# Kernel optimization log

Hardware: AMD Instinct MI355X
Metric: run time of the kernel (lower is better)

## Reference

```python
import jax, jax.numpy as jnp
import numpy as np

WH, WW = 7, 7
N = WH * WW
DIM = 384
HEADS = 12
NW = 64          # windows per image
B_ = 2048        # batch * NW


def _relative_position_index():
    ch, cw = np.meshgrid(np.arange(WH), np.arange(WW), indexing='ij')
    coords = np.stack([ch, cw]).reshape(2, -1)                      # [2, N]
    rel = coords[:, :, None] - coords[:, None, :]                   # [2, N, N]
    rel = rel.transpose(1, 2, 0)
    rel[:, :, 0] += WH - 1
    rel[:, :, 1] += WW - 1
    rel[:, :, 0] *= 2 * WW - 1
    return jnp.asarray(rel.sum(-1), dtype=jnp.int32)                # [N, N]


def setup_inputs() -> dict:
    key = jax.random.key(0)
    ks = jax.random.split(key, 7)
    return {
        'x': jax.random.normal(ks[0], (B_, N, DIM), dtype=jnp.float32),
        'qkv_w': jax.random.normal(ks[1], (3 * DIM, DIM), dtype=jnp.float32) * 0.02,
        'qkv_b': jax.random.normal(ks[2], (3 * DIM,), dtype=jnp.float32) * 0.02,
        'proj_w': jax.random.normal(ks[3], (DIM, DIM), dtype=jnp.float32) * 0.02,
        'proj_b': jax.random.normal(ks[4], (DIM,), dtype=jnp.float32) * 0.02,
        'bias_table': jax.random.normal(ks[5], ((2 * WH - 1) * (2 * WW - 1), HEADS), dtype=jnp.float32) * 0.02,
        'mask': jax.random.normal(ks[6], (NW, N, N), dtype=jnp.float32),
        'rel_idx': _relative_position_index(),
    }


def reference(x, qkv_w, qkv_b, proj_w, proj_b, bias_table, mask, rel_idx):
    B_, n, C = x.shape
    H = HEADS
    hd = C // H
    scale = hd ** (-0.5)

    qkv = x @ qkv_w.T + qkv_b                                        # [B_, N, 3C]
    qkv = qkv.reshape(B_, n, 3, H, hd).transpose(2, 0, 3, 1, 4)      # [3, B_, H, N, hd]
    q, k, v = qkv[0], qkv[1], qkv[2]

    attn = jnp.einsum('bhqd,bhkd->bhqk', q * scale, k)               # [B_, H, N, N]

    rpb = bias_table[rel_idx.reshape(-1)].reshape(n, n, H)           # gather [N, N, H]
    attn = attn + rpb.transpose(2, 0, 1)[None]                       # [B_, H, N, N]

    nW = mask.shape[0]
    attn = attn.reshape(B_ // nW, nW, H, n, n) + mask[None, :, None]
    attn = attn.reshape(B_, H, n, n)
    attn = jax.nn.softmax(attn, axis=-1)

    out = jnp.einsum('bhqk,bhkd->bhqd', attn, v)                     # [B_, H, N, hd]
    out = out.transpose(0, 2, 1, 3).reshape(B_, n, C)
    return out @ proj_w.T + proj_b
```

## Files before the change

kernel.cpp:

```cpp
#include <hip/hip_runtime.h>
#include <hip/hip_bf16.h>
#include <cstdint>
#include <cstddef>

#define NTOK 49
#define DIM 384
#define KDIM 384
#define HEADS 12
#define HD 32
#define BATCH 2048
#define MROWS (BATCH * NTOK)

typedef unsigned short u16;
typedef __bf16 bf16x8 __attribute__((ext_vector_type(8)));
typedef unsigned short u16x8 __attribute__((ext_vector_type(8)));
typedef float f32x4 __attribute__((ext_vector_type(4)));

__device__ __forceinline__ u16 f2b(float f) {
  union { float f; unsigned u; } v; v.f = f;
  unsigned r = v.u + 0x7fffu + ((v.u >> 16) & 1u);
  return (u16)(r >> 16);
}

__device__ __forceinline__ bf16x8 ld_bf8(const u16* p) {
  u16x8 u = *(const u16x8*)p;
  return __builtin_bit_cast(bf16x8, u);
}

__device__ __forceinline__ void gload_lds16(const void* g, void* l) {
  __builtin_amdgcn_global_load_lds(
      (const __attribute__((address_space(1))) unsigned*)g,
      (__attribute__((address_space(3))) unsigned*)l, 16, 0, 0);
}

__global__ __launch_bounds__(256) void k_prep(const float* __restrict__ x,
                                              u16* __restrict__ xb,
                                              const float* __restrict__ qkv_w,
                                              u16* __restrict__ wqkvb,
                                              const float* __restrict__ proj_w,
                                              u16* __restrict__ wprojb,
                                              const float* __restrict__ bias_table,
                                              const float* __restrict__ mask,
                                              const int* __restrict__ rel_idx,
                                              float* __restrict__ rpbm) {
  int blk = blockIdx.x;
  if (blk < 38208) {
    const float* in;
    u16* out;
    int i;
    if (blk < 37632) {
      in = x; out = xb; i = blk * 256 + threadIdx.x;
    } else if (blk < 38064) {
      in = qkv_w; out = wqkvb; i = (blk - 37632) * 256 + threadIdx.x;
    } else {
      in = proj_w; out = wprojb; i = (blk - 38064) * 256 + threadIdx.x;
    }
    float4 v = ((const float4*)in)[i];
    ushort4 o;
    o.x = f2b(v.x); o.y = f2b(v.y); o.z = f2b(v.z); o.w = f2b(v.w);
    ((ushort4*)out)[i] = o;
  } else {
    int idx = (blk - 38208) * 256 + threadIdx.x;
    int r  = idx & 3;
    int l  = (idx >> 2) & 63;
    int ni = (idx >> 8) & 3;
    int mi = (idx >> 10) & 3;
    int w  = (idx >> 12) & 63;
    int h  = idx >> 18;
    int row = mi * 16 + (l >> 4) * 4 + r;
    int col = ni * 16 + (l & 15);
    float v = -1e30f;
    if (row < NTOK && col < NTOK)
      v = bias_table[rel_idx[row * NTOK + col] * HEADS + h] +
          mask[(w * NTOK + row) * NTOK + col];
    rpbm[idx] = v;
  }
}

template <int OUT_BF16, int NCOLS, int NTN, int GD8>
__global__ __launch_bounds__(512, 4) void k_gemm256(const u16* __restrict__ A,
                                                    const u16* __restrict__ B,
                                                    const float* __restrict__ bias,
                                                    void* __restrict__ Cv) {
  __shared__ u16 sh[36864];
  int bid = blockIdx.x;
  int tile = (bid & 7) * GD8 + (bid >> 3);
  int mt = tile / NTN, nt = tile - mt * NTN;
  long m0 = (long)mt * 256;
  int n0 = nt * 128;
  int tid = threadIdx.x;
  int lane = tid & 63, wid = tid >> 6;
  int wr = (wid >> 1) * 64, wc = (wid & 1) * 64;
  int c = lane & 15, g = lane >> 4;
  int gsw = (g ^ ((c >> 1) & 3)) * 8;

  int srow = wid * 16 + (lane >> 2);
  int scol = ((lane & 3) ^ ((lane >> 3) & 3)) * 8;
  const u16* gA = A + (m0 + srow) * (long)KDIM + scol;
  const u16* gB = B + (long)(n0 + srow) * KDIM + scol;
  int lrow = srow, lseg = (lane & 3) * 8;

  f32x4 acc[4][4] = {};
  bf16x8 af[4], bfr[4];

#define STAGE256(BUF, KT)                                                      \
  {                                                                            \
    u16* As_ = sh + (BUF) * 12288;                                             \
    u16* Bs_ = As_ + 8192;                                                     \
    gload_lds16(gA + (KT), &As_[lrow * 32 + lseg]);                            \
    gload_lds16(gA + (KT) + 128L * KDIM, &As_[(lrow + 128) * 32 + lseg]);      \
    gload_lds16(gB + (KT), &Bs_[lrow * 32 + lseg]);                            \
  }

#define FRAGREAD(BUF)                                                          \
  {                                                                            \
    const u16* As = sh + (BUF) * 12288;                                        \
    const u16* Bs = As + 8192;                                                 \
    _Pragma("unroll") for (int i = 0; i < 4; ++i) {                            \
      af[i]  = ld_bf8(&As[(wr + i * 16 + c) * 32 + gsw]);                      \
      bfr[i] = ld_bf8(&Bs[(wc + i * 16 + c) * 32 + gsw]);                      \
    }                                                                          \
  }

#define MFMA_CL                                                                \
  __builtin_amdgcn_s_setprio(1);                                               \
  _Pragma("unroll") for (int mi = 0; mi < 4; ++mi)                             \
  _Pragma("unroll") for (int ni = 0; ni < 4; ++ni)                             \
      acc[mi][ni] = __builtin_amdgcn_mfma_f32_16x16x32_bf16(                   \
          af[mi], bfr[ni], acc[mi][ni], 0, 0, 0);                              \
  __builtin_amdgcn_s_setprio(0);

#define GITER(T, NV)                                                           \
  {                                                                            \
    MFMA_CL;                                                                   \
    asm volatile("s_waitcnt vmcnt(" #NV ")" ::: "memory");                     \
    __builtin_amdgcn_s_barrier();                                              \
    __builtin_amdgcn_sched_barrier(0);                                         \
    if ((T) + 3 < 12) STAGE256((T) % 3, ((T) + 3) * 32);                       \
    FRAGREAD(((T) + 1) % 3);                                                   \
  }

  STAGE256(0, 0);
  STAGE256(1, 32);
  STAGE256(2, 64);
  asm volatile("s_waitcnt vmcnt(6)" ::: "memory");
  __builtin_amdgcn_s_barrier();
  __builtin_amdgcn_sched_barrier(0);
  FRAGREAD(0);

  GITER(0, 3)  GITER(1, 3)  GITER(2, 3)  GITER(3, 3)
  GITER(4, 3)  GITER(5, 3)  GITER(6, 3)  GITER(7, 3)
  GITER(8, 3)  GITER(9, 3)  GITER(10, 0)
  { MFMA_CL; }
  __builtin_amdgcn_s_barrier();
#undef GITER
#undef MFMA_CL
#undef FRAGREAD
#undef STAGE256

  if (OUT_BF16) {
    u16* C = (u16*)Cv;
#pragma unroll
    for (int mi = 0; mi < 4; ++mi)
#pragma unroll
      for (int ni = 0; ni < 4; ++ni) {
        int col = wc + ni * 16 + c;
        float bv = bias[n0 + col];
#pragma unroll
        for (int r = 0; r < 4; ++r) {
          int row = wr + mi * 16 + g * 4 + r;
          sh[row * 128 + col] = f2b(acc[mi][ni][r] + bv);
        }
      }
    __syncthreads();
#pragma unroll
    for (int rep = 0; rep < 8; ++rep) {
      int idx = rep * 4096 + tid * 8;
      int row = idx >> 7, col = idx & 127;
      *(u16x8*)(C + (m0 + row) * NCOLS + n0 + col) = *(const u16x8*)&sh[idx];
    }
  } else {
    float* C = (float*)Cv;
    float* shf = (float*)sh;
#pragma unroll
    for (int chunk = 0; chunk < 2; ++chunk) {
      __syncthreads();
      if ((wid >> 2) == chunk) {
#pragma unroll
        for (int mi = 0; mi < 4; ++mi)
#pragma unroll
          for (int ni = 0; ni < 4; ++ni) {
            int col = wc + ni * 16 + c;
            float bv = bias[n0 + col];
#pragma unroll
            for (int r = 0; r < 4; ++r) {
              int lr = ((wid >> 1) & 1) * 64 + mi * 16 + g * 4 + r;
              shf[lr * 128 + col] = acc[mi][ni][r] + bv;
            }
          }
      }
      __syncthreads();
#pragma unroll
      for (int rep = 0; rep < 8; ++rep) {
        int idx = rep * 2048 + tid * 4;
        int row = idx >> 7, col = idx & 127;
        *(float4*)(C + (m0 + chunk * 128 + row) * NCOLS + n0 + col) =
            *(const float4*)&shf[idx];
      }
    }
  }
}

__global__ __launch_bounds__(256) void k_attn(const u16* __restrict__ qkv,
                                              const float* __restrict__ rpbm,
                                              u16* __restrict__ attnout) {
  __shared__ u16 P_lds[4][64 * 64];
  __shared__ u16 vT_lds[4][32 * 64];
  int lane = threadIdx.x & 63, wid = threadIdx.x >> 6;
  int blk = blockIdx.x;
  int w = blk / 96;
  int rr = blk - w * 96;
  int j = rr / 3;
  int hb = rr - j * 3;
  int b = j * 64 + w;
  int h = hb * 4 + wid;
  const u16* base = qkv + (size_t)b * (NTOK * 1152);
  int c = lane & 15, g = lane >> 4;

  u16* vt = vT_lds[wid];
  {
    const u16* vbase = base + 2 * DIM + h * HD;
#pragma unroll
    for (int t = 0; t < 4; ++t) {
      int idx = t * 64 + lane;
      int jj = idx >> 2, d0 = (idx & 3) * 8;
      int jr = jj < NTOK ? jj : NTOK - 1;
      u16x8 vv = *(const u16x8*)(vbase + (size_t)jr * 1152 + d0);
#pragma unroll
      for (int dd = 0; dd < 8; ++dd) {
        int d = d0 + dd;
        int byte = (d * 128 + jj * 2) ^ ((d & 7) << 4);
        *(u16*)((char*)vt + byte) = (u16)vv[dd];
      }
    }
  }

  bf16x8 qa[4], kb[4];
#pragma unroll
  for (int mi = 0; mi < 4; ++mi) {
    int row = mi * 16 + c; if (row > NTOK - 1) row = NTOK - 1;
    qa[mi] = ld_bf8(base + (size_t)row * 1152 + h * HD + g * 8);
  }
#pragma unroll
  for (int ni = 0; ni < 4; ++ni) {
    int row = ni * 16 + c; if (row > NTOK - 1) row = NTOK - 1;
    kb[ni] = ld_bf8(base + (size_t)row * 1152 + DIM + h * HD + g * 8);
  }

  f32x4 s[4][4] = {};
#pragma unroll
  for (int mi = 0; mi < 4; ++mi)
#pragma unroll
    for (int ni = 0; ni < 4; ++ni)
      s[mi][ni] = __builtin_amdgcn_mfma_f32_16x16x32_bf16(qa[mi], kb[ni],
                                                          s[mi][ni], 0, 0, 0);

  const float scale = 0.17677669529663687f;
  const f32x4* rp = (const f32x4*)(rpbm + ((size_t)(h * 64 + w)) * 4096);
#pragma unroll
  for (int mi = 0; mi < 4; ++mi)
#pragma unroll
    for (int ni = 0; ni < 4; ++ni) {
      f32x4 rv = rp[(mi * 4 + ni) * 64 + lane];
#pragma unroll
      for (int r = 0; r < 4; ++r)
        s[mi][ni][r] = s[mi][ni][r] * scale + rv[r];
    }

#pragma unroll
  for (int mi = 0; mi < 4; ++mi)
#pragma unroll
    for (int r = 0; r < 4; ++r) {
      float mx = fmaxf(fmaxf(s[mi][0][r], s[mi][1][r]),
                       fmaxf(s[mi][2][r], s[mi][3][r]));
      mx = fmaxf(mx, __shfl_xor(mx, 1));
      mx = fmaxf(mx, __shfl_xor(mx, 2));
      mx = fmaxf(mx, __shfl_xor(mx, 4));
      mx = fmaxf(mx, __shfl_xor(mx, 8));
      float sum = 0.f;
#pragma unroll
      for (int ni = 0; ni < 4; ++ni) {
        float p = __expf(s[mi][ni][r] - mx);
        s[mi][ni][r] = p;
        sum += p;
      }
      sum += __shfl_xor(sum, 1);
      sum += __shfl_xor(sum, 2);
      sum += __shfl_xor(sum, 4);
      sum += __shfl_xor(sum, 8);
      float inv = __builtin_amdgcn_rcpf(sum);
#pragma unroll
      for (int ni = 0; ni < 4; ++ni) s[mi][ni][r] *= inv;
    }

  u16* pl = P_lds[wid];
#pragma unroll
  for (int mi = 0; mi < 4; ++mi)
#pragma unroll
    for (int ni = 0; ni < 4; ++ni) {
      int col = ni * 16 + c;
#pragma unroll
      for (int r = 0; r < 4; ++r) {
        int row = mi * 16 + g * 4 + r;
        int byte = (row * 128 + col * 2) ^ ((row & 7) << 4);
        *(u16*)((char*)pl + byte) = f2b(s[mi][ni][r]);
      }
    }
  asm volatile("s_waitcnt lgkmcnt(0)" ::: "memory");

  f32x4 o[4][2] = {};
#pragma unroll
  for (int ks = 0; ks < 2; ++ks) {
    bf16x8 vb[2];
#pragma unroll
    for (int n2 = 0; n2 < 2; ++n2) {
      int d = n2 * 16 + c;
      int byte = (d * 128 + ks * 64 + g * 16) ^ ((d & 7) << 4);
      vb[n2] = __builtin_bit_cast(bf16x8, *(const u16x8*)((const char*)vt + byte));
    }
#pragma unroll
    for (int mi = 0; mi < 4; ++mi) {
      int row = mi * 16 + c;
      int byte = (row * 128 + ks * 64 + g * 16) ^ ((row & 7) << 4);
      bf16x8 pa = __builtin_bit_cast(bf16x8, *(const u16x8*)((const char*)pl + byte));
#pragma unroll
      for (int n2 = 0; n2 < 2; ++n2)
        o[mi][n2] = __builtin_amdgcn_mfma_f32_16x16x32_bf16(pa, vb[n2],
                                                            o[mi][n2], 0, 0, 0);
    }
  }

  u16* obase = attnout + (size_t)b * (NTOK * DIM) + h * HD;
#pragma unroll
  for (int mi = 0; mi < 4; ++mi)
#pragma unroll
    for (int r = 0; r < 4; ++r) {
      int row = mi * 16 + g * 4 + r;
      if (row < NTOK) {
#pragma unroll
        for (int n2 = 0; n2 < 2; ++n2)
          obase[(size_t)row * DIM + n2 * 16 + c] = f2b(o[mi][n2][r]);
      }
    }
}

extern "C" void kernel_launch(void* const* d_in, const int* in_sizes, int n_in,
                              void* d_out, int out_size, void* d_ws, size_t ws_size,
                              hipStream_t stream) {
  const float* x       = (const float*)d_in[0];
  const float* qkv_w   = (const float*)d_in[1];
  const float* qkv_b   = (const float*)d_in[2];
  const float* proj_w  = (const float*)d_in[3];
  const float* proj_b  = (const float*)d_in[4];
  const float* bias_tb = (const float*)d_in[5];
  const float* mask    = (const float*)d_in[6];
  const int*   rel_idx = (const int*)d_in[7];
  float* out = (float*)d_out;

  char* ws = (char*)d_ws;
  u16*   xb      = (u16*)(ws + 0);
  u16*   wqkvb   = (u16*)(ws + 77070336);
  u16*   wprojb  = (u16*)(ws + 77955072);
  float* rpbm    = (float*)(ws + 78249984);
  u16*   qkv     = (u16*)(ws + 90832896);
  u16*   attnout = (u16*)(ws + 322043904);

  k_prep<<<50496, 256, 0, stream>>>(x, xb, qkv_w, wqkvb, proj_w, wprojb,
                                    bias_tb, mask, rel_idx, rpbm);

  k_gemm256<1, 1152, 9, 441><<<3528, 512, 0, stream>>>(xb, wqkvb, qkv_b,
                                                       (void*)qkv);

  k_attn<<<6144, 256, 0, stream>>>(qkv, rpbm, attnout);

  k_gemm256<0, 384, 3, 147><<<1176, 512, 0, stream>>>(attnout, wprojb, proj_b,
                                                      (void*)out);

  (void)in_sizes; (void)n_in; (void)out_size; (void)ws_size;
}
```

Before: 342.3 us.

## Compute transposed attention scores to cut softmax shuffles and defer normalization

The attention kernel now computes S^T = K·Q^T, so each query's scores sit along a lane's registers rather than across 16 lanes. The row max and sum then need only two cross-lane shuffles instead of four. The precomputed bias+mask tensor is stored transposed to match. Probabilities are packed to bf16 with v_cvt_pk_bf16_f32 and written as 8-byte LDS stores, and the 1/sum normalization moves to after the PV product, where it is applied once per output element. The PV MFMA is reoriented as V^T·P^T, so output stores become scattered 2-byte writes along the head dimension.

Result: no change. 341.7 us (-0.2%).

```diff
diff --git a/kernel.cpp b/kernel.cpp
--- a/kernel.cpp
+++ b/kernel.cpp
@@ -67,12 +67,12 @@
     int mi = (idx >> 10) & 3;
     int w  = (idx >> 12) & 63;
     int h  = idx >> 18;
-    int row = mi * 16 + (l >> 4) * 4 + r;
-    int col = ni * 16 + (l & 15);
+    int kk = mi * 16 + (l >> 4) * 4 + r;
+    int qq = ni * 16 + (l & 15);
     float v = -1e30f;
-    if (row < NTOK && col < NTOK)
-      v = bias_table[rel_idx[row * NTOK + col] * HEADS + h] +
-          mask[(w * NTOK + row) * NTOK + col];
+    if (kk < NTOK && qq < NTOK)
+      v = bias_table[rel_idx[qq * NTOK + kk] * HEADS + h] +
+          mask[(w * NTOK + qq) * NTOK + kk];
     rpbm[idx] = v;
   }
 }
@@ -212,7 +212,7 @@
 }
 
 __global__ __launch_bounds__(256) void k_attn(const u16* __restrict__ qkv,
-                                              const float* __restrict__ rpbm,
+                                              const float* __restrict__ rpbmT,
                                               u16* __restrict__ attnout) {
   __shared__ u16 P_lds[4][64 * 64];
   __shared__ u16 vT_lds[4][32 * 64];
@@ -245,111 +245,115 @@
     }
   }
 
-  bf16x8 qa[4], kb[4];
+  bf16x8 kf[4], qf[4];
 #pragma unroll
   for (int mi = 0; mi < 4; ++mi) {
     int row = mi * 16 + c; if (row > NTOK - 1) row = NTOK - 1;
-    qa[mi] = ld_bf8(base + (size_t)row * 1152 + h * HD + g * 8);
-  }
-#pragma unroll
-  for (int ni = 0; ni < 4; ++ni) {
-    int row = ni * 16 + c; if (row > NTOK - 1) row = NTOK - 1;
-    kb[ni] = ld_bf8(base + (size_t)row * 1152 + DIM + h * HD + g * 8);
-  }
-
-  f32x4 s[4][4] = {};
+    kf[mi] = ld_bf8(base + (size_t)row * 1152 + DIM + h * HD + g * 8);
+  }
+#pragma unroll
+  for (int nj = 0; nj < 4; ++nj) {
+    int row = nj * 16 + c; if (row > NTOK - 1) row = NTOK - 1;
+    qf[nj] = ld_bf8(base + (size_t)row * 1152 + h * HD + g * 8);
+  }
+
+  f32x4 s[4][4];
+  f32x4 zf = {0.f, 0.f, 0.f, 0.f};
 #pragma unroll
   for (int mi = 0; mi < 4; ++mi)
 #pragma unroll
-    for (int ni = 0; ni < 4; ++ni)
-      s[mi][ni] = __builtin_amdgcn_mfma_f32_16x16x32_bf16(qa[mi], kb[ni],
-                                                          s[mi][ni], 0, 0, 0);
+    for (int nj = 0; nj < 4; ++nj)
+      s[mi][nj] = __builtin_amdgcn_mfma_f32_16x16x32_bf16(kf[mi], qf[nj], zf,
+                                                          0, 0, 0);
 
   const float scale = 0.17677669529663687f;
-  const f32x4* rp = (const f32x4*)(rpbm + ((size_t)(h * 64 + w)) * 4096);
+  const f32x4* rp = (const f32x4*)(rpbmT + ((size_t)(h * 64 + w)) * 4096);
 #pragma unroll
   for (int mi = 0; mi < 4; ++mi)
 #pragma unroll
-    for (int ni = 0; ni < 4; ++ni) {
-      f32x4 rv = rp[(mi * 4 + ni) * 64 + lane];
+    for (int nj = 0; nj < 4; ++nj) {
+      f32x4 rv = rp[(mi * 4 + nj) * 64 + lane];
 #pragma unroll
       for (int r = 0; r < 4; ++r)
-        s[mi][ni][r] = s[mi][ni][r] * scale + rv[r];
-    }
-
+        s[mi][nj][r] = s[mi][nj][r] * scale + rv[r];
+    }
+
+  float inv[4];
+#pragma unroll
+  for (int nj = 0; nj < 4; ++nj) {
+    float mx = s[0][nj][0];
+#pragma unroll
+    for (int mi = 0; mi < 4; ++mi)
+#pragma unroll
+      for (int r = 0; r < 4; ++r)
+        mx = fmaxf(mx, s[mi][nj][r]);
+    mx = fmaxf(mx, __shfl_xor(mx, 16));
+    mx = fmaxf(mx, __shfl_xor(mx, 32));
+    float sum = 0.f;
+#pragma unroll
+    for (int mi = 0; mi < 4; ++mi)
+#pragma unroll
+      for (int r = 0; r < 4; ++r) {
+        float p = __expf(s[mi][nj][r] - mx);
+        s[mi][nj][r] = p;
+        sum += p;
+      }
+    sum += __shfl_xor(sum, 16);
+    sum += __shfl_xor(sum, 32);
+    inv[nj] = __builtin_amdgcn_rcpf(sum);
+  }
+
+  u16* pl = P_lds[wid];
 #pragma unroll
   for (int mi = 0; mi < 4; ++mi)
 #pragma unroll
-    for (int r = 0; r < 4; ++r) {
-      float mx = fmaxf(fmaxf(s[mi][0][r], s[mi][1][r]),
-                       fmaxf(s[mi][2][r], s[mi][3][r]));
-      mx = fmaxf(mx, __shfl_xor(mx, 1));
-      mx = fmaxf(mx, __shfl_xor(mx, 2));
-      mx = fmaxf(mx, __shfl_xor(mx, 4));
-      mx = fmaxf(mx, __shfl_xor(mx, 8));
-      float sum = 0.f;
-#pragma unroll
-      for (int ni = 0; ni < 4; ++ni) {
-        float p = __expf(s[mi][ni][r] - mx);
-        s[mi][ni][r] = p;
-        sum += p;
-      }
-      sum += __shfl_xor(sum, 1);
-      sum += __shfl_xor(sum, 2);
-      sum += __shfl_xor(sum, 4);
-      sum += __shfl_xor(sum, 8);
-      float inv = __builtin_amdgcn_rcpf(sum);
-#pragma unroll
-      for (int ni = 0; ni < 4; ++ni) s[mi][ni][r] *= inv;
-    }
-
-  u16* pl = P_lds[wid];
-#pragma unroll
-  for (int mi = 0; mi < 4; ++mi)
-#pragma unroll
-    for (int ni = 0; ni < 4; ++ni) {
-      int col = ni * 16 + c;
-#pragma unroll
-      for (int r = 0; r < 4; ++r) {
-        int row = mi * 16 + g * 4 + r;
-        int byte = (row * 128 + col * 2) ^ ((row & 7) << 4);
-        *(u16*)((char*)pl + byte) = f2b(s[mi][ni][r]);
-      }
+    for (int nj = 0; nj < 4; ++nj) {
+      unsigned w0, w1;
+      asm("v_cvt_pk_bf16_f32 %0, %1, %2"
+          : "=v"(w0) : "v"(s[mi][nj][0]), "v"(s[mi][nj][1]));
+      asm("v_cvt_pk_bf16_f32 %0, %1, %2"
+          : "=v"(w1) : "v"(s[mi][nj][2]), "v"(s[mi][nj][3]));
+      int q = nj * 16 + c;
+      int byte = (q * 128 + (mi * 16 + g * 4) * 2) ^ ((c & 7) << 4);
+      uint2 val; val.x = w0; val.y = w1;
+      *(uint2*)((char*)pl + byte) = val;
     }
   asm volatile("s_waitcnt lgkmcnt(0)" ::: "memory");
-
-  f32x4 o[4][2] = {};
+  __builtin_amdgcn_sched_barrier(0);
+
+  f32x4 o[2][4] = {};
 #pragma unroll
   for (int ks = 0; ks < 2; ++ks) {
     bf16x8 vb[2];
 #pragma unroll
-    for (int n2 = 0; n2 < 2; ++n2) {
-      int d = n2 * 16 + c;
+    for (int mi2 = 0; mi2 < 2; ++mi2) {
+      int d = mi2 * 16 + c;
       int byte = (d * 128 + ks * 64 + g * 16) ^ ((d & 7) << 4);
-      vb[n2] = __builtin_bit_cast(bf16x8, *(const u16x8*)((const char*)vt + byte));
-    }
-#pragma unroll
-    for (int mi = 0; mi < 4; ++mi) {
-      int row = mi * 16 + c;
-      int byte = (row * 128 + ks * 64 + g * 16) ^ ((row & 7) << 4);
-      bf16x8 pa = __builtin_bit_cast(bf16x8, *(const u16x8*)((const char*)pl + byte));
-#pragma unroll
-      for (int n2 = 0; n2 < 2; ++n2)
-        o[mi][n2] = __builtin_amdgcn_mfma_f32_16x16x32_bf16(pa, vb[n2],
-                                                            o[mi][n2], 0, 0, 0);
+      vb[mi2] = __builtin_bit_cast(bf16x8, *(const u16x8*)((const char*)vt + byte));
+    }
+#pragma unroll
+    for (int nj = 0; nj < 4; ++nj) {
+      int q = nj * 16 + c;
+      int byte = (q * 128 + (ks * 32 + g * 8) * 2) ^ ((c & 7) << 4);
+      bf16x8 pb = __builtin_bit_cast(bf16x8, *(const u16x8*)((const char*)pl + byte));
+#pragma unroll
+      for (int mi2 = 0; mi2 < 2; ++mi2)
+        o[mi2][nj] = __builtin_amdgcn_mfma_f32_16x16x32_bf16(vb[mi2], pb,
+                                                             o[mi2][nj], 0, 0, 0);
     }
   }
 
   u16* obase = attnout + (size_t)b * (NTOK * DIM) + h * HD;
 #pragma unroll
-  for (int mi = 0; mi < 4; ++mi)
-#pragma unroll
-    for (int r = 0; r < 4; ++r) {
-      int row = mi * 16 + g * 4 + r;
-      if (row < NTOK) {
-#pragma unroll
-        for (int n2 = 0; n2 < 2; ++n2)
-          obase[(size_t)row * DIM + n2 * 16 + c] = f2b(o[mi][n2][r]);
+  for (int mi2 = 0; mi2 < 2; ++mi2)
+#pragma unroll
+    for (int nj = 0; nj < 4; ++nj) {
+      int q = nj * 16 + c;
+      if (q < NTOK) {
+#pragma unroll
+        for (int r = 0; r < 4; ++r)
+          obase[(size_t)q * DIM + mi2 * 16 + g * 4 + r] =
+              f2b(o[mi2][nj][r] * inv[nj]);
       }
     }
 }
```
